# Kernel optimization log

Measured on AMD Instinct MI355X. Metric: run time of the kernel, lower is better.

Reference implementation:

```python
import jax, jax.numpy as jnp
import numpy as np

TOP_K = 2


def setup_inputs() -> dict:
    key = jax.random.key(0)
    ks = jax.random.split(key, 5)
    B, S, H, F, E = 1, 2048, 1024, 3584, 8
    scale_h = 1.0 / np.sqrt(H)
    scale_f = 1.0 / np.sqrt(F)
    return {
        "hidden_states": jax.random.normal(ks[0], (B, S, H), dtype=jnp.float32),
        "gate_w": jax.random.normal(ks[1], (E, H), dtype=jnp.float32) * scale_h,
        "w1": jax.random.normal(ks[2], (E, H, F), dtype=jnp.float32) * scale_h,
        "w3": jax.random.normal(ks[3], (E, H, F), dtype=jnp.float32) * scale_h,
        "w2": jax.random.normal(ks[4], (E, F, H), dtype=jnp.float32) * scale_f,
    }


def reference(hidden_states, gate_w, w1, w2, w3):
    B, S, H = hidden_states.shape
    E = gate_w.shape[0]
    x = hidden_states.reshape(-1, H)  # [T, H]
    # Router: logits -> fp32 softmax -> top-k -> renormalize
    router_logits = x @ gate_w.T  # [T, E]
    probs = jax.nn.softmax(router_logits.astype(jnp.float32), axis=-1)
    top_w, top_idx = jax.lax.top_k(probs, TOP_K)  # [T, K]
    top_w = top_w / jnp.sum(top_w, axis=-1, keepdims=True)
    top_w = top_w.astype(x.dtype)
    # Dense combine weights [T, E]: routing weight if expert selected else 0
    combine = jnp.sum(jax.nn.one_hot(top_idx, E, dtype=x.dtype) * top_w[..., None], axis=1)
    # Per-expert SwiGLU FFN, weighted-summed (loop over small fixed E)
    out = jnp.zeros_like(x)
    for e in range(E):
        h = jax.nn.silu(x @ w1[e]) * (x @ w3[e])  # [T, F]
        out = out + (h @ w2[e]) * combine[:, e:e + 1]
    return out.reshape(B, S, H), router_logits
```

## Files before the change

### kernel.cpp

```cpp
#include <hip/hip_runtime.h>
#include <cstdint>
#include <cstddef>

#define Tt 2048
#define Hh 1024
#define Ff 3584
#define Ee 8
#define ROWS_CAP 5120

#define OFF_CTRL   0u
#define OFF_TOKE   256u
#define OFF_TOKW   (256u + 16384u)
#define OFF_ROWMAP (256u + 32768u)
#define OFF_ROWW   (256u + 32768u + 20480u)
#define OFF_XG     (1ull << 20)
#define OFF_G      (12ull << 20)
#define OFF_W1T    (48ull << 20)
#define OFF_W3T    (104ull << 20)
#define OFF_W2T    (160ull << 20)

typedef __attribute__((ext_vector_type(8))) short bf16x8;
typedef __attribute__((ext_vector_type(4))) float f32x4;

__device__ __forceinline__ unsigned short f2bf(float f) {
  unsigned int u = __float_as_uint(f);
  u += 0x7fffu + ((u >> 16) & 1u);
  return (unsigned short)(u >> 16);
}

__device__ __forceinline__ void gload_lds16(const void* g, void* l) {
  auto gp = (const __attribute__((address_space(1))) char*)(uintptr_t)g;
  auto lp = (__attribute__((address_space(3))) char*)(uintptr_t)l;
  __builtin_amdgcn_global_load_lds(gp, lp, 16, 0, 0);
}

__device__ __forceinline__ bf16x8 frg(const char* lds, int row, int gc) {
  return *(const bf16x8*)(lds + row * 64 + ((gc ^ ((row >> 1) & 3)) * 16));
}

__global__ __launch_bounds__(256) void router_kernel(
    const float* __restrict__ x, const float* __restrict__ gw,
    float* __restrict__ logits_out, int* __restrict__ tok_e,
    float* __restrict__ tok_w, int* __restrict__ ctrl) {
  const int lane = threadIdx.x & 63;
  const int t = blockIdx.x * 4 + (threadIdx.x >> 6);
  const float4* xp = (const float4*)(x + (size_t)t * Hh + lane * 16);
  float4 x0 = xp[0], x1 = xp[1], x2 = xp[2], x3 = xp[3];
  float lg[Ee];
#pragma unroll
  for (int e = 0; e < Ee; ++e) {
    const float4* gp = (const float4*)(gw + e * Hh + lane * 16);
    float4 g0 = gp[0], g1 = gp[1], g2 = gp[2], g3 = gp[3];
    float s = x0.x*g0.x + x0.y*g0.y + x0.z*g0.z + x0.w*g0.w
            + x1.x*g1.x + x1.y*g1.y + x1.z*g1.z + x1.w*g1.w
            + x2.x*g2.x + x2.y*g2.y + x2.z*g2.z + x2.w*g2.w
            + x3.x*g3.x + x3.y*g3.y + x3.z*g3.z + x3.w*g3.w;
#pragma unroll
    for (int o = 32; o; o >>= 1) s += __shfl_xor(s, o);
    lg[e] = s;
  }
  if (lane == 0) {
    float m = lg[0];
#pragma unroll
    for (int e = 1; e < Ee; ++e) m = fmaxf(m, lg[e]);
    float p[Ee];
#pragma unroll
    for (int e = 0; e < Ee; ++e) p[e] = expf(lg[e] - m);
    int a0 = 0;
#pragma unroll
    for (int e = 1; e < Ee; ++e) if (p[e] > p[a0]) a0 = e;
    int a1 = (a0 == 0) ? 1 : 0;
#pragma unroll
    for (int e = 0; e < Ee; ++e) if (e != a0 && p[e] > p[a1]) a1 = e;
    float rs = p[a0] + p[a1];
    float w0 = p[a0] / rs, w1 = p[a1] / rs;
#pragma unroll
    for (int e = 0; e < Ee; ++e) logits_out[(size_t)t * Ee + e] = lg[e];
    tok_e[t * 2] = a0; tok_e[t * 2 + 1] = a1;
    tok_w[t * 2] = w0; tok_w[t * 2 + 1] = w1;
    atomicAdd(&ctrl[a0], 1); atomicAdd(&ctrl[a1], 1);
  }
}

__global__ void offsets_kernel(int* ctrl) {
  if (threadIdx.x == 0) {
    int acc = 0;
    for (int e = 0; e < Ee; ++e) {
      ctrl[16 + e] = acc;
      acc += ((ctrl[e] + 127) >> 7) << 7;
    }
    ctrl[16 + Ee] = acc;
  }
}

__global__ __launch_bounds__(512) void assign_kernel(
    int* ctrl, const int* __restrict__ tok_e, const float* __restrict__ tok_w,
    int* __restrict__ rowmap, float* __restrict__ roww) {
  int i = blockIdx.x * 512 + threadIdx.x;
  if (i < 2 * Tt) {
    int e = tok_e[i];
    int pos = atomicAdd(&ctrl[8 + e], 1);
    int r = ctrl[16 + e] + pos;
    rowmap[r] = i >> 1;
    roww[r] = tok_w[i];
  }
  if (i < Ee * 128) {
    int e = i >> 7, pd = i & 127;
    int o = ctrl[16 + e], o1 = ctrl[16 + e + 1], c = ctrl[e];
    int r = o + c + pd;
    if (r < o1) { rowmap[r] = -1; roww[r] = 0.f; }
  }
}

__global__ __launch_bounds__(128) void gather_kernel(
    const float* __restrict__ x, const int* __restrict__ ctrl,
    const int* __restrict__ rowmap, unsigned short* __restrict__ Xg) {
  int r = blockIdx.x;
  if (r >= ctrl[16 + Ee]) return;
  int t = rowmap[r];
  int j = threadIdx.x;
  uint4 v = make_uint4(0u, 0u, 0u, 0u);
  if (t >= 0) {
    const float4* xp = (const float4*)(x + (size_t)t * Hh + j * 8);
    float4 a = xp[0], b = xp[1];
    v.x = (unsigned)f2bf(a.x) | ((unsigned)f2bf(a.y) << 16);
    v.y = (unsigned)f2bf(a.z) | ((unsigned)f2bf(a.w) << 16);
    v.z = (unsigned)f2bf(b.x) | ((unsigned)f2bf(b.y) << 16);
    v.w = (unsigned)f2bf(b.z) | ((unsigned)f2bf(b.w) << 16);
  }
  *(uint4*)(Xg + (size_t)r * Hh + j * 8) = v;
}

__global__ __launch_bounds__(256) void tc_all(
    const float* __restrict__ w1, const float* __restrict__ w3,
    const float* __restrict__ w2, unsigned short* __restrict__ w1T,
    unsigned short* __restrict__ w3T, unsigned short* __restrict__ w2T) {
  __shared__ unsigned short sT[64 * 72];
  const int z = blockIdx.z;
  const float* in = (z == 0) ? w1 : (z == 1) ? w3 : w2;
  unsigned short* out = (z == 0) ? w1T : (z == 1) ? w3T : w2T;
  const int C = (z == 2) ? Hh : Ff;
  const int tiles_c = (z == 2) ? 16 : 56;
  const int R = (z == 2) ? Ff : Hh;
  const int e = blockIdx.y;
  const int tr = blockIdx.x / tiles_c, tc = blockIdx.x % tiles_c;
  const int r0 = tr * 64, c0 = tc * 64;
  const float* src = in + (size_t)e * R * C;
  unsigned short* dst = out + (size_t)e * R * C;
  const int t = threadIdx.x;
#pragma unroll
  for (int p = 0; p < 4; ++p) {
    int row = p * 16 + (t >> 4);
    float4 v = *(const float4*)(src + (size_t)(r0 + row) * C + c0 + (t & 15) * 4);
    int cl = (t & 15) * 4;
    sT[(cl + 0) * 72 + row] = f2bf(v.x);
    sT[(cl + 1) * 72 + row] = f2bf(v.y);
    sT[(cl + 2) * 72 + row] = f2bf(v.z);
    sT[(cl + 3) * 72 + row] = f2bf(v.w);
  }
  __syncthreads();
  const int oc = t >> 2, half = t & 3;
  uint4 u0 = *(const uint4*)&sT[oc * 72 + half * 16];
  uint4 u1 = *(const uint4*)&sT[oc * 72 + half * 16 + 8];
  unsigned short* op = dst + (size_t)(c0 + oc) * R + r0 + half * 16;
  *(uint4*)op = u0;
  *(uint4*)(op + 8) = u1;
}

__global__ __launch_bounds__(512, 4) void ffn13_bf16(
    const unsigned short* __restrict__ Xg, const unsigned short* __restrict__ w1T,
    const unsigned short* __restrict__ w3T, const int* __restrict__ ctrl,
    unsigned short* __restrict__ G) {
  __shared__ alignas(16) char sA[2][8192], sB1[2][8192], sB3[2][8192];
  int lin = blockIdx.y * 28 + blockIdx.x;
  int wg = (lin & 7) * 448 + (lin >> 3);
  int bx = wg % 28, by = wg / 28;
  const int e = by >> 4, mt = by & 15;
  const int off0 = ctrl[16 + e], off1 = ctrl[16 + e + 1];
  const int row0 = off0 + mt * 128;
  if (row0 >= off1) return;
  const int n0 = bx * 128;
  const int tid = threadIdx.x, lane = tid & 63, wv = tid >> 6;
  const int wr = wv >> 2, wc = wv & 3;
  const unsigned short* w1e = w1T + (size_t)e * Ff * Hh;
  const unsigned short* w3e = w3T + (size_t)e * Ff * Hh;
  f32x4 acc1[4][2] = {};
  f32x4 acc3[4][2] = {};
  const int srow = wv * 16 + (lane >> 2);
  const int sgc = (lane & 3) ^ ((lane >> 3) & 3);
  const int swb = wv * 16;

  {
    size_t so = (size_t)sgc * 8;
    gload_lds16(Xg + (size_t)(row0 + srow) * Hh + so, sA[0] + swb * 64);
    gload_lds16(w1e + (size_t)(n0 + srow) * Hh + so, sB1[0] + swb * 64);
    gload_lds16(w3e + (size_t)(n0 + srow) * Hh + so, sB3[0] + swb * 64);
  }
  __syncthreads();
  for (int it = 0; it < 32; ++it) {
    int cur = it & 1;
    if (it < 31) {
      size_t so = (size_t)(it + 1) * 32 + sgc * 8;
      gload_lds16(Xg + (size_t)(row0 + srow) * Hh + so, sA[cur ^ 1] + swb * 64);
      gload_lds16(w1e + (size_t)(n0 + srow) * Hh + so, sB1[cur ^ 1] + swb * 64);
      gload_lds16(w3e + (size_t)(n0 + srow) * Hh + so, sB3[cur ^ 1] + swb * 64);
    }
    const int gc = lane >> 4;
    bf16x8 af[4];
#pragma unroll
    for (int mi = 0; mi < 4; ++mi)
      af[mi] = frg(sA[cur], wr * 64 + mi * 16 + (lane & 15), gc);
    __builtin_amdgcn_s_setprio(1);
#pragma unroll
    for (int ni = 0; ni < 2; ++ni) {
      bf16x8 b1 = frg(sB1[cur], wc * 32 + ni * 16 + (lane & 15), gc);
      bf16x8 b3 = frg(sB3[cur], wc * 32 + ni * 16 + (lane & 15), gc);
#pragma unroll
      for (int mi = 0; mi < 4; ++mi) {
        acc1[mi][ni] = __builtin_amdgcn_mfma_f32_16x16x32_bf16(af[mi], b1, acc1[mi][ni], 0, 0, 0);
        acc3[mi][ni] = __builtin_amdgcn_mfma_f32_16x16x32_bf16(af[mi], b3, acc3[mi][ni], 0, 0, 0);
      }
    }
    __builtin_amdgcn_s_setprio(0);
    __syncthreads();
  }
  const int rb = wr * 64 + 4 * (lane >> 4), cb = wc * 32 + (lane & 15);
#pragma unroll
  for (int mi = 0; mi < 4; ++mi)
#pragma unroll
    for (int ni = 0; ni < 2; ++ni)
#pragma unroll
      for (int r = 0; r < 4; ++r) {
        float h1 = acc1[mi][ni][r], h3 = acc3[mi][ni][r];
        float gv = h1 / (1.f + __expf(-h1)) * h3;
        G[(size_t)(row0 + rb + mi * 16 + r) * Ff + n0 + cb + ni * 16] = f2bf(gv);
      }
}

__global__ __launch_bounds__(256, 4) void ffn2_bf16(
    const unsigned short* __restrict__ G, const unsigned short* __restrict__ w2T,
    const int* __restrict__ ctrl, const int* __restrict__ rowmap,
    const float* __restrict__ roww, float* __restrict__ out) {
  __shared__ alignas(16) char sA[2][8192], sB[2][8192];
  int lin = blockIdx.y * 8 + blockIdx.x;
  int wg = (lin & 7) * 128 + (lin >> 3);
  int bx = wg % 8, by = wg / 8;
  const int e = by >> 4, mt = by & 15;
  const int off0 = ctrl[16 + e], off1 = ctrl[16 + e + 1];
  const int row0 = off0 + mt * 128;
  if (row0 >= off1) return;
  const int n0 = bx * 128;
  const int kb = blockIdx.z * (Ff / 4);
  const int tid = threadIdx.x, lane = tid & 63, wv = tid >> 6;
  const int wr = wv >> 1, wc = wv & 1;
  const unsigned short* w2e = w2T + (size_t)e * Ff * Hh;
  f32x4 acc[4][4] = {};
  const int sl = lane >> 2;
  const int sgc = (lane & 3) ^ ((lane >> 3) & 3);

#pragma unroll
  for (int half = 0; half < 2; ++half) {
    int wb = wv * 16 + half * 64;
    size_t so = (size_t)kb + sgc * 8;
    gload_lds16(G + (size_t)(row0 + wb + sl) * Ff + so, sA[0] + wb * 64);
    gload_lds16(w2e + (size_t)(n0 + wb + sl) * Ff + so, sB[0] + wb * 64);
  }
  __syncthreads();
  for (int it = 0; it < 28; ++it) {
    int cur = it & 1;
    if (it < 27) {
#pragma unroll
      for (int half = 0; half < 2; ++half) {
        int wb = wv * 16 + half * 64;
        size_t so = (size_t)kb + (it + 1) * 32 + sgc * 8;
        gload_lds16(G + (size_t)(row0 + wb + sl) * Ff + so, sA[cur ^ 1] + wb * 64);
        gload_lds16(w2e + (size_t)(n0 + wb + sl) * Ff + so, sB[cur ^ 1] + wb * 64);
      }
    }
    const int gc = lane >> 4;
    bf16x8 af[4];
#pragma unroll
    for (int mi = 0; mi < 4; ++mi)
      af[mi] = frg(sA[cur], wr * 64 + mi * 16 + (lane & 15), gc);
    __builtin_amdgcn_s_setprio(1);
#pragma unroll
    for (int ni = 0; ni < 4; ++ni) {
      bf16x8 b = frg(sB[cur], wc * 64 + ni * 16 + (lane & 15), gc);
#pragma unroll
      for (int mi = 0; mi < 4; ++mi)
        acc[mi][ni] = __builtin_amdgcn_mfma_f32_16x16x32_bf16(af[mi], b, acc[mi][ni], 0, 0, 0);
    }
    __builtin_amdgcn_s_setprio(0);
    __syncthreads();
  }
  const int rb = wr * 64 + 4 * (lane >> 4), cb = wc * 64 + (lane & 15);
#pragma unroll
  for (int mi = 0; mi < 4; ++mi)
#pragma unroll
    for (int r = 0; r < 4; ++r) {
      int grow = row0 + rb + mi * 16 + r;
      int t = rowmap[grow];
      if (t < 0) continue;
      float wgt = roww[grow];
#pragma unroll
      for (int ni = 0; ni < 4; ++ni)
        atomicAdd(&out[(size_t)t * Hh + n0 + cb + ni * 16], wgt * acc[mi][ni][r]);
    }
}

extern "C" void kernel_launch(void* const* d_in, const int* in_sizes, int n_in,
                              void* d_out, int out_size, void* d_ws, size_t ws_size,
                              hipStream_t stream) {
  const float* x  = (const float*)d_in[0];
  const float* gw = (const float*)d_in[1];
  const float* w1 = (const float*)d_in[2];
  const float* w3 = (const float*)d_in[3];
  const float* w2 = (const float*)d_in[4];
  float* out = (float*)d_out;
  float* logits = out + (size_t)Tt * Hh;
  char* ws = (char*)d_ws;
  int* ctrl = (int*)(ws + OFF_CTRL);
  int* tok_e = (int*)(ws + OFF_TOKE);
  float* tok_w = (float*)(ws + OFF_TOKW);
  int* rowmap = (int*)(ws + OFF_ROWMAP);
  float* roww = (float*)(ws + OFF_ROWW);
  unsigned short* Xg = (unsigned short*)(ws + OFF_XG);
  unsigned short* G  = (unsigned short*)(ws + OFF_G);
  unsigned short* w1T = (unsigned short*)(ws + OFF_W1T);
  unsigned short* w3T = (unsigned short*)(ws + OFF_W3T);
  unsigned short* w2T = (unsigned short*)(ws + OFF_W2T);

  hipMemsetAsync(ctrl, 0, 256, stream);
  hipMemsetAsync(out, 0, (size_t)Tt * Hh * sizeof(float), stream);
  router_kernel<<<Tt / 4, 256, 0, stream>>>(x, gw, logits, tok_e, tok_w, ctrl);
  offsets_kernel<<<1, 64, 0, stream>>>(ctrl);
  assign_kernel<<<8, 512, 0, stream>>>(ctrl, tok_e, tok_w, rowmap, roww);
  gather_kernel<<<ROWS_CAP, 128, 0, stream>>>(x, ctrl, rowmap, Xg);
  tc_all<<<dim3(896, Ee, 3), 256, 0, stream>>>(w1, w3, w2, w1T, w3T, w2T);
  ffn13_bf16<<<dim3(28, Ee * 16), 512, 0, stream>>>(Xg, w1T, w3T, ctrl, G);
  ffn2_bf16<<<dim3(8, Ee * 16, 4), 256, 0, stream>>>(G, w2T, ctrl, rowmap, roww, out);
}
```

Before: 372.8 us.

## Use partial vmcnt waits in GEMM loops and swizzle transpose LDS tile

The GEMM main loops of both FFN kernels now issue next-tile async global-to-LDS loads before waiting. They wait only with a partial s_waitcnt vmcnt so the current tile's loads complete while the prefetch stays in flight. Full __syncthreads are replaced by raw s_barrier plus sched_barrier, and the last iteration issues a dummy wraparound prefetch to keep the loop branch-free. Separately, the weight transpose kernel packs four rows per thread into 8-byte LDS stores with an XOR swizzle, cutting scalar 2-byte shared stores and bank conflicts. The risk is subtle ordering bugs and extra wasted loads at loop end.

```diff
diff --git a/kernel.cpp b/kernel.cpp
--- a/kernel.cpp
+++ b/kernel.cpp
@@ -135,7 +135,7 @@
     const float* __restrict__ w1, const float* __restrict__ w3,
     const float* __restrict__ w2, unsigned short* __restrict__ w1T,
     unsigned short* __restrict__ w3T, unsigned short* __restrict__ w2T) {
-  __shared__ unsigned short sT[64 * 72];
+  __shared__ alignas(16) char sT[64 * 128];
   const int z = blockIdx.z;
   const float* in = (z == 0) ? w1 : (z == 1) ? w3 : w2;
   unsigned short* out = (z == 0) ? w1T : (z == 1) ? w3T : w2T;
@@ -148,23 +148,35 @@
   const float* src = in + (size_t)e * R * C;
   unsigned short* dst = out + (size_t)e * R * C;
   const int t = threadIdx.x;
-#pragma unroll
-  for (int p = 0; p < 4; ++p) {
-    int row = p * 16 + (t >> 4);
-    float4 v = *(const float4*)(src + (size_t)(r0 + row) * C + c0 + (t & 15) * 4);
-    int cl = (t & 15) * 4;
-    sT[(cl + 0) * 72 + row] = f2bf(v.x);
-    sT[(cl + 1) * 72 + row] = f2bf(v.y);
-    sT[(cl + 2) * 72 + row] = f2bf(v.z);
-    sT[(cl + 3) * 72 + row] = f2bf(v.w);
+
+  const int col4 = (t & 15) * 4, rb = (t >> 4) * 4;
+  float4 v0 = *(const float4*)(src + (size_t)(r0 + rb + 0) * C + c0 + col4);
+  float4 v1 = *(const float4*)(src + (size_t)(r0 + rb + 1) * C + c0 + col4);
+  float4 v2 = *(const float4*)(src + (size_t)(r0 + rb + 2) * C + c0 + col4);
+  float4 v3 = *(const float4*)(src + (size_t)(r0 + rb + 3) * C + c0 + col4);
+  const float* a0 = (const float*)&v0;
+  const float* a1 = (const float*)&v1;
+  const float* a2 = (const float*)&v2;
+  const float* a3 = (const float*)&v3;
+#pragma unroll
+  for (int j = 0; j < 4; ++j) {
+    int c = col4 + j;
+    int M = (((c & 7) ^ ((c >> 3) & 7)) << 4);
+    uint2 val;
+    val.x = (unsigned)f2bf(a0[j]) | ((unsigned)f2bf(a1[j]) << 16);
+    val.y = (unsigned)f2bf(a2[j]) | ((unsigned)f2bf(a3[j]) << 16);
+    *(uint2*)(sT + c * 128 + ((rb * 2) ^ M)) = val;
   }
   __syncthreads();
-  const int oc = t >> 2, half = t & 3;
-  uint4 u0 = *(const uint4*)&sT[oc * 72 + half * 16];
-  uint4 u1 = *(const uint4*)&sT[oc * 72 + half * 16 + 8];
-  unsigned short* op = dst + (size_t)(c0 + oc) * R + r0 + half * 16;
-  *(uint4*)op = u0;
-  *(uint4*)(op + 8) = u1;
+  const int lane = t & 63, wv = t >> 6;
+  const int h8 = lane >> 3;
+#pragma unroll
+  for (int p = 0; p < 2; ++p) {
+    int c = p * 32 + wv * 8 + (lane & 7);
+    int M = (((c & 7) ^ ((c >> 3) & 7)) << 4);
+    uint4 q = *(const uint4*)(sT + c * 128 + ((h8 * 16) ^ M));
+    *(uint4*)(dst + (size_t)(c0 + c) * R + r0 + h8 * 8) = q;
+  }
 }
 
 __global__ __launch_bounds__(512, 4) void ffn13_bf16(
@@ -190,21 +202,24 @@
   const int sgc = (lane & 3) ^ ((lane >> 3) & 3);
   const int swb = wv * 16;
 
-  {
-    size_t so = (size_t)sgc * 8;
-    gload_lds16(Xg + (size_t)(row0 + srow) * Hh + so, sA[0] + swb * 64);
-    gload_lds16(w1e + (size_t)(n0 + srow) * Hh + so, sB1[0] + swb * 64);
-    gload_lds16(w3e + (size_t)(n0 + srow) * Hh + so, sB3[0] + swb * 64);
-  }
-  __syncthreads();
+  const unsigned short* gA = Xg + (size_t)(row0 + srow) * Hh + sgc * 8;
+  const unsigned short* gB1 = w1e + (size_t)(n0 + srow) * Hh + sgc * 8;
+  const unsigned short* gB3 = w3e + (size_t)(n0 + srow) * Hh + sgc * 8;
+
+  gload_lds16(gA, sA[0] + swb * 64);
+  gload_lds16(gB1, sB1[0] + swb * 64);
+  gload_lds16(gB3, sB3[0] + swb * 64);
+
   for (int it = 0; it < 32; ++it) {
     int cur = it & 1;
-    if (it < 31) {
-      size_t so = (size_t)(it + 1) * 32 + sgc * 8;
-      gload_lds16(Xg + (size_t)(row0 + srow) * Hh + so, sA[cur ^ 1] + swb * 64);
-      gload_lds16(w1e + (size_t)(n0 + srow) * Hh + so, sB1[cur ^ 1] + swb * 64);
-      gload_lds16(w3e + (size_t)(n0 + srow) * Hh + so, sB3[cur ^ 1] + swb * 64);
-    }
+    int nx = it + 1; if (nx == 32) nx = 0;
+    size_t so = (size_t)nx * 32;
+    gload_lds16(gA + so, sA[cur ^ 1] + swb * 64);
+    gload_lds16(gB1 + so, sB1[cur ^ 1] + swb * 64);
+    gload_lds16(gB3 + so, sB3[cur ^ 1] + swb * 64);
+    asm volatile("s_waitcnt vmcnt(3)" ::: "memory");
+    __builtin_amdgcn_s_barrier();
+    __builtin_amdgcn_sched_barrier(0);
     const int gc = lane >> 4;
     bf16x8 af[4];
 #pragma unroll
@@ -222,8 +237,10 @@
       }
     }
     __builtin_amdgcn_s_setprio(0);
-    __syncthreads();
-  }
+    __builtin_amdgcn_sched_barrier(0);
+    __builtin_amdgcn_s_barrier();
+  }
+  asm volatile("s_waitcnt vmcnt(0)" ::: "memory");
   const int rb = wr * 64 + 4 * (lane >> 4), cb = wc * 32 + (lane & 15);
 #pragma unroll
   for (int mi = 0; mi < 4; ++mi)
@@ -258,25 +275,27 @@
   const int sl = lane >> 2;
   const int sgc = (lane & 3) ^ ((lane >> 3) & 3);
 
-#pragma unroll
-  for (int half = 0; half < 2; ++half) {
-    int wb = wv * 16 + half * 64;
-    size_t so = (size_t)kb + sgc * 8;
-    gload_lds16(G + (size_t)(row0 + wb + sl) * Ff + so, sA[0] + wb * 64);
-    gload_lds16(w2e + (size_t)(n0 + wb + sl) * Ff + so, sB[0] + wb * 64);
-  }
-  __syncthreads();
+  const unsigned short* gA0 = G + (size_t)(row0 + wv * 16 + sl) * Ff + kb + sgc * 8;
+  const unsigned short* gA1 = G + (size_t)(row0 + 64 + wv * 16 + sl) * Ff + kb + sgc * 8;
+  const unsigned short* gB0 = w2e + (size_t)(n0 + wv * 16 + sl) * Ff + kb + sgc * 8;
+  const unsigned short* gB1 = w2e + (size_t)(n0 + 64 + wv * 16 + sl) * Ff + kb + sgc * 8;
+
+  gload_lds16(gA0, sA[0] + (wv * 16) * 64);
+  gload_lds16(gA1, sA[0] + (wv * 16 + 64) * 64);
+  gload_lds16(gB0, sB[0] + (wv * 16) * 64);
+  gload_lds16(gB1, sB[0] + (wv * 16 + 64) * 64);
+
   for (int it = 0; it < 28; ++it) {
     int cur = it & 1;
-    if (it < 27) {
-#pragma unroll
-      for (int half = 0; half < 2; ++half) {
-        int wb = wv * 16 + half * 64;
-        size_t so = (size_t)kb + (it + 1) * 32 + sgc * 8;
-        gload_lds16(G + (size_t)(row0 + wb + sl) * Ff + so, sA[cur ^ 1] + wb * 64);
-        gload_lds16(w2e + (size_t)(n0 + wb + sl) * Ff + so, sB[cur ^ 1] + wb * 64);
-      }
-    }
+    int nx = it + 1; if (nx == 28) nx = 0;
+    size_t so = (size_t)nx * 32;
+    gload_lds16(gA0 + so, sA[cur ^ 1] + (wv * 16) * 64);
+    gload_lds16(gA1 + so, sA[cur ^ 1] + (wv * 16 + 64) * 64);
+    gload_lds16(gB0 + so, sB[cur ^ 1] + (wv * 16) * 64);
+    gload_lds16(gB1 + so, sB[cur ^ 1] + (wv * 16 + 64) * 64);
+    asm volatile("s_waitcnt vmcnt(4)" ::: "memory");
+    __builtin_amdgcn_s_barrier();
+    __builtin_amdgcn_sched_barrier(0);
     const int gc = lane >> 4;
     bf16x8 af[4];
 #pragma unroll
@@ -291,8 +310,10 @@
         acc[mi][ni] = __builtin_amdgcn_mfma_f32_16x16x32_bf16(af[mi], b, acc[mi][ni], 0, 0, 0);
     }
     __builtin_amdgcn_s_setprio(0);
-    __syncthreads();
-  }
+    __builtin_amdgcn_sched_barrier(0);
+    __builtin_amdgcn_s_barrier();
+  }
+  asm volatile("s_waitcnt vmcnt(0)" ::: "memory");
   const int rb = wr * 64 + 4 * (lane >> 4), cb = wc * 64 + (lane & 15);
 #pragma unroll
   for (int mi = 0; mi < 4; ++mi)
```

Measured after the change: 367.1 us. No clear change (-1.5%).

## Fuse fp32 weight conversion into expert GEMMs and drop transpose pass

Applied to the files above, without the earlier changes.

Removes the separate kernel that converted and transposed all expert weights to bf16 each call. Both FFN GEMMs now read fp32 weights straight from the original layout, pack them to bf16 in registers with v_cvt_pk_bf16_f32, and store them into swizzled LDS while the current tile's MFMAs run. The down-projection also drops its 4-way K split: it runs 512 threads with 112 K iterations and half as many output columns per wave. This saves a full read-and-write pass over the weights, at the cost of strided fp32 global loads and more weight traffic from reloads across M tiles and less parallelism in the second GEMM.

```diff
diff --git a/kernel.cpp b/kernel.cpp
--- a/kernel.cpp
+++ b/kernel.cpp
@@ -15,9 +15,6 @@
 #define OFF_ROWW   (256u + 32768u + 20480u)
 #define OFF_XG     (1ull << 20)
 #define OFF_G      (12ull << 20)
-#define OFF_W1T    (48ull << 20)
-#define OFF_W3T    (104ull << 20)
-#define OFF_W2T    (160ull << 20)
 
 typedef __attribute__((ext_vector_type(8))) short bf16x8;
 typedef __attribute__((ext_vector_type(4))) float f32x4;
@@ -26,6 +23,12 @@
   unsigned int u = __float_as_uint(f);
   u += 0x7fffu + ((u >> 16) & 1u);
   return (unsigned short)(u >> 16);
+}
+
+__device__ __forceinline__ unsigned pkbf(float a, float b) {
+  unsigned r;
+  asm("v_cvt_pk_bf16_f32 %0, %1, %2" : "=v"(r) : "v"(a), "v"(b));
+  return r;
 }
 
 __device__ __forceinline__ void gload_lds16(const void* g, void* l) {
@@ -131,45 +134,9 @@
   *(uint4*)(Xg + (size_t)r * Hh + j * 8) = v;
 }
 
-__global__ __launch_bounds__(256) void tc_all(
-    const float* __restrict__ w1, const float* __restrict__ w3,
-    const float* __restrict__ w2, unsigned short* __restrict__ w1T,
-    unsigned short* __restrict__ w3T, unsigned short* __restrict__ w2T) {
-  __shared__ unsigned short sT[64 * 72];
-  const int z = blockIdx.z;
-  const float* in = (z == 0) ? w1 : (z == 1) ? w3 : w2;
-  unsigned short* out = (z == 0) ? w1T : (z == 1) ? w3T : w2T;
-  const int C = (z == 2) ? Hh : Ff;
-  const int tiles_c = (z == 2) ? 16 : 56;
-  const int R = (z == 2) ? Ff : Hh;
-  const int e = blockIdx.y;
-  const int tr = blockIdx.x / tiles_c, tc = blockIdx.x % tiles_c;
-  const int r0 = tr * 64, c0 = tc * 64;
-  const float* src = in + (size_t)e * R * C;
-  unsigned short* dst = out + (size_t)e * R * C;
-  const int t = threadIdx.x;
-#pragma unroll
-  for (int p = 0; p < 4; ++p) {
-    int row = p * 16 + (t >> 4);
-    float4 v = *(const float4*)(src + (size_t)(r0 + row) * C + c0 + (t & 15) * 4);
-    int cl = (t & 15) * 4;
-    sT[(cl + 0) * 72 + row] = f2bf(v.x);
-    sT[(cl + 1) * 72 + row] = f2bf(v.y);
-    sT[(cl + 2) * 72 + row] = f2bf(v.z);
-    sT[(cl + 3) * 72 + row] = f2bf(v.w);
-  }
-  __syncthreads();
-  const int oc = t >> 2, half = t & 3;
-  uint4 u0 = *(const uint4*)&sT[oc * 72 + half * 16];
-  uint4 u1 = *(const uint4*)&sT[oc * 72 + half * 16 + 8];
-  unsigned short* op = dst + (size_t)(c0 + oc) * R + r0 + half * 16;
-  *(uint4*)op = u0;
-  *(uint4*)(op + 8) = u1;
-}
-
-__global__ __launch_bounds__(512, 4) void ffn13_bf16(
-    const unsigned short* __restrict__ Xg, const unsigned short* __restrict__ w1T,
-    const unsigned short* __restrict__ w3T, const int* __restrict__ ctrl,
+__global__ __launch_bounds__(512, 4) void ffn13_fused(
+    const unsigned short* __restrict__ Xg, const float* __restrict__ w1,
+    const float* __restrict__ w3, const int* __restrict__ ctrl,
     unsigned short* __restrict__ G) {
   __shared__ alignas(16) char sA[2][8192], sB1[2][8192], sB3[2][8192];
   int lin = blockIdx.y * 28 + blockIdx.x;
@@ -182,28 +149,47 @@
   const int n0 = bx * 128;
   const int tid = threadIdx.x, lane = tid & 63, wv = tid >> 6;
   const int wr = wv >> 2, wc = wv & 3;
-  const unsigned short* w1e = w1T + (size_t)e * Ff * Hh;
-  const unsigned short* w3e = w3T + (size_t)e * Ff * Hh;
+  const float* w1e = w1 + (size_t)e * Hh * Ff;
+  const float* w3e = w3 + (size_t)e * Hh * Ff;
   f32x4 acc1[4][2] = {};
   f32x4 acc3[4][2] = {};
   const int srow = wv * 16 + (lane >> 2);
   const int sgc = (lane & 3) ^ ((lane >> 3) & 3);
-  const int swb = wv * 16;
-
+  const unsigned short* gA = Xg + (size_t)(row0 + srow) * Hh + sgc * 8;
+  const int bn = tid & 127, bkq = tid >> 7;
+  const int posB = bkq ^ ((bn >> 1) & 3);
+  const int wofB = bn * 64 + posB * 16;
+  const float* pB1 = w1e + (size_t)(bkq * 8) * Ff + n0 + bn;
+  const float* pB3 = w3e + (size_t)(bkq * 8) * Ff + n0 + bn;
+  float r1[8], r3[8];
+
+#pragma unroll
+  for (int i = 0; i < 8; ++i) r1[i] = pB1[(size_t)i * Ff];
+#pragma unroll
+  for (int i = 0; i < 8; ++i) r3[i] = pB3[(size_t)i * Ff];
+  gload_lds16(gA, sA[0] + wv * 1024);
   {
-    size_t so = (size_t)sgc * 8;
-    gload_lds16(Xg + (size_t)(row0 + srow) * Hh + so, sA[0] + swb * 64);
-    gload_lds16(w1e + (size_t)(n0 + srow) * Hh + so, sB1[0] + swb * 64);
-    gload_lds16(w3e + (size_t)(n0 + srow) * Hh + so, sB3[0] + swb * 64);
+    uint4 q;
+    q.x = pkbf(r1[0], r1[1]); q.y = pkbf(r1[2], r1[3]);
+    q.z = pkbf(r1[4], r1[5]); q.w = pkbf(r1[6], r1[7]);
+    *(uint4*)(sB1[0] + wofB) = q;
+    q.x = pkbf(r3[0], r3[1]); q.y = pkbf(r3[2], r3[3]);
+    q.z = pkbf(r3[4], r3[5]); q.w = pkbf(r3[6], r3[7]);
+    *(uint4*)(sB3[0] + wofB) = q;
   }
   __syncthreads();
+
   for (int it = 0; it < 32; ++it) {
-    int cur = it & 1;
+    const int cur = it & 1;
     if (it < 31) {
-      size_t so = (size_t)(it + 1) * 32 + sgc * 8;
-      gload_lds16(Xg + (size_t)(row0 + srow) * Hh + so, sA[cur ^ 1] + swb * 64);
-      gload_lds16(w1e + (size_t)(n0 + srow) * Hh + so, sB1[cur ^ 1] + swb * 64);
-      gload_lds16(w3e + (size_t)(n0 + srow) * Hh + so, sB3[cur ^ 1] + swb * 64);
+      const size_t ko = (size_t)(it + 1) * 32;
+      gload_lds16(gA + ko, sA[cur ^ 1] + wv * 1024);
+      const float* p1 = pB1 + ko * Ff;
+      const float* p3 = pB3 + ko * Ff;
+#pragma unroll
+      for (int i = 0; i < 8; ++i) r1[i] = p1[(size_t)i * Ff];
+#pragma unroll
+      for (int i = 0; i < 8; ++i) r3[i] = p3[(size_t)i * Ff];
     }
     const int gc = lane >> 4;
     bf16x8 af[4];
@@ -222,6 +208,15 @@
       }
     }
     __builtin_amdgcn_s_setprio(0);
+    if (it < 31) {
+      uint4 q;
+      q.x = pkbf(r1[0], r1[1]); q.y = pkbf(r1[2], r1[3]);
+      q.z = pkbf(r1[4], r1[5]); q.w = pkbf(r1[6], r1[7]);
+      *(uint4*)(sB1[cur ^ 1] + wofB) = q;
+      q.x = pkbf(r3[0], r3[1]); q.y = pkbf(r3[2], r3[3]);
+      q.z = pkbf(r3[4], r3[5]); q.w = pkbf(r3[6], r3[7]);
+      *(uint4*)(sB3[cur ^ 1] + wofB) = q;
+    }
     __syncthreads();
   }
   const int rb = wr * 64 + 4 * (lane >> 4), cb = wc * 32 + (lane & 15);
@@ -237,8 +232,8 @@
       }
 }
 
-__global__ __launch_bounds__(256, 4) void ffn2_bf16(
-    const unsigned short* __restrict__ G, const unsigned short* __restrict__ w2T,
+__global__ __launch_bounds__(512, 4) void ffn2_fused(
+    const unsigned short* __restrict__ G, const float* __restrict__ w2,
     const int* __restrict__ ctrl, const int* __restrict__ rowmap,
     const float* __restrict__ roww, float* __restrict__ out) {
   __shared__ alignas(16) char sA[2][8192], sB[2][8192];
@@ -250,32 +245,38 @@
   const int row0 = off0 + mt * 128;
   if (row0 >= off1) return;
   const int n0 = bx * 128;
-  const int kb = blockIdx.z * (Ff / 4);
   const int tid = threadIdx.x, lane = tid & 63, wv = tid >> 6;
-  const int wr = wv >> 1, wc = wv & 1;
-  const unsigned short* w2e = w2T + (size_t)e * Ff * Hh;
-  f32x4 acc[4][4] = {};
-  const int sl = lane >> 2;
+  const int wr = wv >> 2, wc = wv & 3;
+  const float* w2e = w2 + (size_t)e * Ff * Hh;
+  f32x4 acc[4][2] = {};
+  const int srow = wv * 16 + (lane >> 2);
   const int sgc = (lane & 3) ^ ((lane >> 3) & 3);
-
-#pragma unroll
-  for (int half = 0; half < 2; ++half) {
-    int wb = wv * 16 + half * 64;
-    size_t so = (size_t)kb + sgc * 8;
-    gload_lds16(G + (size_t)(row0 + wb + sl) * Ff + so, sA[0] + wb * 64);
-    gload_lds16(w2e + (size_t)(n0 + wb + sl) * Ff + so, sB[0] + wb * 64);
+  const unsigned short* gA = G + (size_t)(row0 + srow) * Ff + sgc * 8;
+  const int bn = tid & 127, bkq = tid >> 7;
+  const int posB = bkq ^ ((bn >> 1) & 3);
+  const int wofB = bn * 64 + posB * 16;
+  const float* pB = w2e + (size_t)(bkq * 8) * Hh + n0 + bn;
+  float r2[8];
+
+#pragma unroll
+  for (int i = 0; i < 8; ++i) r2[i] = pB[(size_t)i * Hh];
+  gload_lds16(gA, sA[0] + wv * 1024);
+  {
+    uint4 q;
+    q.x = pkbf(r2[0], r2[1]); q.y = pkbf(r2[2], r2[3]);
+    q.z = pkbf(r2[4], r2[5]); q.w = pkbf(r2[6], r2[7]);
+    *(uint4*)(sB[0] + wofB) = q;
   }
   __syncthreads();
-  for (int it = 0; it < 28; ++it) {
-    int cur = it & 1;
-    if (it < 27) {
-#pragma unroll
-      for (int half = 0; half < 2; ++half) {
-        int wb = wv * 16 + half * 64;
-        size_t so = (size_t)kb + (it + 1) * 32 + sgc * 8;
-        gload_lds16(G + (size_t)(row0 + wb + sl) * Ff + so, sA[cur ^ 1] + wb * 64);
-        gload_lds16(w2e + (size_t)(n0 + wb + sl) * Ff + so, sB[cur ^ 1] + wb * 64);
-      }
+
+  for (int it = 0; it < 112; ++it) {
+    const int cur = it & 1;
+    if (it < 111) {
+      const size_t ko = (size_t)(it + 1) * 32;
+      gload_lds16(gA + ko, sA[cur ^ 1] + wv * 1024);
+      const float* p2 = pB + ko * Hh;
+#pragma unroll
+      for (int i = 0; i < 8; ++i) r2[i] = p2[(size_t)i * Hh];
     }
     const int gc = lane >> 4;
     bf16x8 af[4];
@@ -284,16 +285,22 @@
       af[mi] = frg(sA[cur], wr * 64 + mi * 16 + (lane & 15), gc);
     __builtin_amdgcn_s_setprio(1);
 #pragma unroll
-    for (int ni = 0; ni < 4; ++ni) {
-      bf16x8 b = frg(sB[cur], wc * 64 + ni * 16 + (lane & 15), gc);
+    for (int ni = 0; ni < 2; ++ni) {
+      bf16x8 b = frg(sB[cur], wc * 32 + ni * 16 + (lane & 15), gc);
 #pragma unroll
       for (int mi = 0; mi < 4; ++mi)
         acc[mi][ni] = __builtin_amdgcn_mfma_f32_16x16x32_bf16(af[mi], b, acc[mi][ni], 0, 0, 0);
     }
     __builtin_amdgcn_s_setprio(0);
+    if (it < 111) {
+      uint4 q;
+      q.x = pkbf(r2[0], r2[1]); q.y = pkbf(r2[2], r2[3]);
+      q.z = pkbf(r2[4], r2[5]); q.w = pkbf(r2[6], r2[7]);
+      *(uint4*)(sB[cur ^ 1] + wofB) = q;
+    }
     __syncthreads();
   }
-  const int rb = wr * 64 + 4 * (lane >> 4), cb = wc * 64 + (lane & 15);
+  const int rb = wr * 64 + 4 * (lane >> 4), cb = wc * 32 + (lane & 15);
 #pragma unroll
   for (int mi = 0; mi < 4; ++mi)
 #pragma unroll
@@ -303,7 +310,7 @@
       if (t < 0) continue;
       float wgt = roww[grow];
 #pragma unroll
-      for (int ni = 0; ni < 4; ++ni)
+      for (int ni = 0; ni < 2; ++ni)
         atomicAdd(&out[(size_t)t * Hh + n0 + cb + ni * 16], wgt * acc[mi][ni][r]);
     }
 }
@@ -326,9 +333,6 @@
   float* roww = (float*)(ws + OFF_ROWW);
   unsigned short* Xg = (unsigned short*)(ws + OFF_XG);
   unsigned short* G  = (unsigned short*)(ws + OFF_G);
-  unsigned short* w1T = (unsigned short*)(ws + OFF_W1T);
-  unsigned short* w3T = (unsigned short*)(ws + OFF_W3T);
-  unsigned short* w2T = (unsigned short*)(ws + OFF_W2T);
 
   hipMemsetAsync(ctrl, 0, 256, stream);
   hipMemsetAsync(out, 0, (size_t)Tt * Hh * sizeof(float), stream);
@@ -336,7 +340,6 @@
   offsets_kernel<<<1, 64, 0, stream>>>(ctrl);
   assign_kernel<<<8, 512, 0, stream>>>(ctrl, tok_e, tok_w, rowmap, roww);
   gather_kernel<<<ROWS_CAP, 128, 0, stream>>>(x, ctrl, rowmap, Xg);
-  tc_all<<<dim3(896, Ee, 3), 256, 0, stream>>>(w1, w3, w2, w1T, w3T, w2T);
-  ffn13_bf16<<<dim3(28, Ee * 16), 512, 0, stream>>>(Xg, w1T, w3T, ctrl, G);
-  ffn2_bf16<<<dim3(8, Ee * 16, 4), 256, 0, stream>>>(G, w2T, ctrl, rowmap, roww, out);
-}
+  ffn13_fused<<<dim3(28, Ee * 16), 512, 0, stream>>>(Xg, w1, w3, ctrl, G);
+  ffn2_fused<<<dim3(8, Ee * 16), 512, 0, stream>>>(G, w2, ctrl, rowmap, roww, out);
+}
```

Result: faster. 344.8 us (-7.5%).

## Compact expert tile schedule, widen weight transpose tiles, retile ffn2 to 512 threads

Applied to the files above, without the earlier changes.

The offsets kernel now builds a compact list of up to 40 (expert, row-tile) pairs, so both GEMMs launch only about 40 row tiles instead of 128 mostly-empty slots with early exits. The weight transpose/convert kernel now handles 128x64 tiles per block, uses packed bf16 conversion and an XOR-swizzled LDS layout, and halves its block count. ffn2 moves to 512 threads with a 32-column warp tile. This removes wasted block launches and scheduling gaps, at the cost of a fixed MAXT cap on row tiles.

```diff
diff --git a/kernel.cpp b/kernel.cpp
--- a/kernel.cpp
+++ b/kernel.cpp
@@ -7,17 +7,18 @@
 #define Ff 3584
 #define Ee 8
 #define ROWS_CAP 5120
+#define MAXT 40
 
 #define OFF_CTRL   0u
-#define OFF_TOKE   256u
-#define OFF_TOKW   (256u + 16384u)
-#define OFF_ROWMAP (256u + 32768u)
-#define OFF_ROWW   (256u + 32768u + 20480u)
-#define OFF_XG     (1ull << 20)
-#define OFF_G      (12ull << 20)
-#define OFF_W1T    (48ull << 20)
-#define OFF_W3T    (104ull << 20)
-#define OFF_W2T    (160ull << 20)
+#define OFF_TOKE   4096u
+#define OFF_TOKW   (4096u + 16384u)
+#define OFF_ROWMAP 65536u
+#define OFF_ROWW   98304u
+#define OFF_XG     262144ull
+#define OFF_G      10747904ull
+#define OFF_W1T    47448064ull
+#define OFF_W3T    106168320ull
+#define OFF_W2T    164888576ull
 
 typedef __attribute__((ext_vector_type(8))) short bf16x8;
 typedef __attribute__((ext_vector_type(4))) float f32x4;
@@ -26,6 +27,12 @@
   unsigned int u = __float_as_uint(f);
   u += 0x7fffu + ((u >> 16) & 1u);
   return (unsigned short)(u >> 16);
+}
+
+__device__ __forceinline__ unsigned pkbf(float a, float b) {
+  unsigned r;
+  asm("v_cvt_pk_bf16_f32 %0, %1, %2" : "=v"(r) : "v"(a), "v"(b));
+  return r;
 }
 
 __device__ __forceinline__ void gload_lds16(const void* g, void* l) {
@@ -90,6 +97,16 @@
       acc += ((ctrl[e] + 127) >> 7) << 7;
     }
     ctrl[16 + Ee] = acc;
+    int idx = 0;
+    for (int e = 0; e < Ee; ++e) {
+      int nt = (ctrl[e] + 127) >> 7;
+      for (int m = 0; m < nt && idx < MAXT; ++m) {
+        ctrl[32 + 2 * idx] = e;
+        ctrl[33 + 2 * idx] = ctrl[16 + e] + m * 128;
+        ++idx;
+      }
+    }
+    for (; idx < MAXT; ++idx) { ctrl[32 + 2 * idx] = 0; ctrl[33 + 2 * idx] = -1; }
   }
 }
 
@@ -135,50 +152,59 @@
     const float* __restrict__ w1, const float* __restrict__ w3,
     const float* __restrict__ w2, unsigned short* __restrict__ w1T,
     unsigned short* __restrict__ w3T, unsigned short* __restrict__ w2T) {
-  __shared__ unsigned short sT[64 * 72];
+  __shared__ alignas(16) char sT[64 * 256];
   const int z = blockIdx.z;
   const float* in = (z == 0) ? w1 : (z == 1) ? w3 : w2;
   unsigned short* out = (z == 0) ? w1T : (z == 1) ? w3T : w2T;
+  const int R = (z == 2) ? Ff : Hh;
   const int C = (z == 2) ? Hh : Ff;
   const int tiles_c = (z == 2) ? 16 : 56;
-  const int R = (z == 2) ? Ff : Hh;
   const int e = blockIdx.y;
-  const int tr = blockIdx.x / tiles_c, tc = blockIdx.x % tiles_c;
-  const int r0 = tr * 64, c0 = tc * 64;
+  const int tr = blockIdx.x / tiles_c, tcc = blockIdx.x % tiles_c;
+  const int r0g = tr * 128, c0 = tcc * 64;
   const float* src = in + (size_t)e * R * C;
   unsigned short* dst = out + (size_t)e * R * C;
   const int t = threadIdx.x;
-#pragma unroll
-  for (int p = 0; p < 4; ++p) {
-    int row = p * 16 + (t >> 4);
-    float4 v = *(const float4*)(src + (size_t)(r0 + row) * C + c0 + (t & 15) * 4);
-    int cl = (t & 15) * 4;
-    sT[(cl + 0) * 72 + row] = f2bf(v.x);
-    sT[(cl + 1) * 72 + row] = f2bf(v.y);
-    sT[(cl + 2) * 72 + row] = f2bf(v.z);
-    sT[(cl + 3) * 72 + row] = f2bf(v.w);
+
+  const int col4 = (t & 15) * 4, rb = (t >> 4) * 8;
+  float4 v[8];
+#pragma unroll
+  for (int i = 0; i < 8; ++i)
+    v[i] = *(const float4*)(src + (size_t)(r0g + rb + i) * C + c0 + col4);
+#pragma unroll
+  for (int j = 0; j < 4; ++j) {
+    const float* a = (const float*)&v[0];
+    int c = col4 + j;
+    int M = (((c & 7) ^ ((c >> 3) & 7)) << 4);
+    uint4 q;
+    q.x = pkbf(((const float*)&v[0])[j], ((const float*)&v[1])[j]);
+    q.y = pkbf(((const float*)&v[2])[j], ((const float*)&v[3])[j]);
+    q.z = pkbf(((const float*)&v[4])[j], ((const float*)&v[5])[j]);
+    q.w = pkbf(((const float*)&v[6])[j], ((const float*)&v[7])[j]);
+    (void)a;
+    *(uint4*)(sT + c * 256 + ((rb * 2) ^ M)) = q;
   }
   __syncthreads();
-  const int oc = t >> 2, half = t & 3;
-  uint4 u0 = *(const uint4*)&sT[oc * 72 + half * 16];
-  uint4 u1 = *(const uint4*)&sT[oc * 72 + half * 16 + 8];
-  unsigned short* op = dst + (size_t)(c0 + oc) * R + r0 + half * 16;
-  *(uint4*)op = u0;
-  *(uint4*)(op + 8) = u1;
-}
-
-__global__ __launch_bounds__(512, 4) void ffn13_bf16(
+  const int oc = t >> 2, part = t & 3;
+  const int M = (((oc & 7) ^ ((oc >> 3) & 7)) << 4);
+#pragma unroll
+  for (int i = 0; i < 4; ++i) {
+    uint4 q = *(const uint4*)(sT + oc * 256 + ((i * 64 + part * 16) ^ M));
+    *(uint4*)(dst + (size_t)(c0 + oc) * R + r0g + i * 32 + part * 8) = q;
+  }
+}
+
+__global__ __launch_bounds__(512, 4) void h13_gemm(
     const unsigned short* __restrict__ Xg, const unsigned short* __restrict__ w1T,
     const unsigned short* __restrict__ w3T, const int* __restrict__ ctrl,
     unsigned short* __restrict__ G) {
   __shared__ alignas(16) char sA[2][8192], sB1[2][8192], sB3[2][8192];
   int lin = blockIdx.y * 28 + blockIdx.x;
-  int wg = (lin & 7) * 448 + (lin >> 3);
-  int bx = wg % 28, by = wg / 28;
-  const int e = by >> 4, mt = by & 15;
-  const int off0 = ctrl[16 + e], off1 = ctrl[16 + e + 1];
-  const int row0 = off0 + mt * 128;
-  if (row0 >= off1) return;
+  int wg = (lin & 7) * 140 + (lin >> 3);
+  int ft = wg % 40, bx = wg / 40;
+  const int e = ctrl[32 + 2 * ft];
+  const int row0 = ctrl[33 + 2 * ft];
+  if (row0 < 0) return;
   const int n0 = bx * 128;
   const int tid = threadIdx.x, lane = tid & 63, wv = tid >> 6;
   const int wr = wv >> 2, wc = wv & 3;
@@ -188,22 +214,22 @@
   f32x4 acc3[4][2] = {};
   const int srow = wv * 16 + (lane >> 2);
   const int sgc = (lane & 3) ^ ((lane >> 3) & 3);
-  const int swb = wv * 16;
-
-  {
-    size_t so = (size_t)sgc * 8;
-    gload_lds16(Xg + (size_t)(row0 + srow) * Hh + so, sA[0] + swb * 64);
-    gload_lds16(w1e + (size_t)(n0 + srow) * Hh + so, sB1[0] + swb * 64);
-    gload_lds16(w3e + (size_t)(n0 + srow) * Hh + so, sB3[0] + swb * 64);
-  }
+  const unsigned short* gA  = Xg  + (size_t)(row0 + srow) * Hh + sgc * 8;
+  const unsigned short* gB1 = w1e + (size_t)(n0 + srow) * Hh + sgc * 8;
+  const unsigned short* gB3 = w3e + (size_t)(n0 + srow) * Hh + sgc * 8;
+
+  gload_lds16(gA,  sA[0]  + wv * 1024);
+  gload_lds16(gB1, sB1[0] + wv * 1024);
+  gload_lds16(gB3, sB3[0] + wv * 1024);
   __syncthreads();
+
   for (int it = 0; it < 32; ++it) {
-    int cur = it & 1;
+    const int cur = it & 1;
     if (it < 31) {
-      size_t so = (size_t)(it + 1) * 32 + sgc * 8;
-      gload_lds16(Xg + (size_t)(row0 + srow) * Hh + so, sA[cur ^ 1] + swb * 64);
-      gload_lds16(w1e + (size_t)(n0 + srow) * Hh + so, sB1[cur ^ 1] + swb * 64);
-      gload_lds16(w3e + (size_t)(n0 + srow) * Hh + so, sB3[cur ^ 1] + swb * 64);
+      const size_t ko = (size_t)(it + 1) * 32;
+      gload_lds16(gA + ko,  sA[cur ^ 1]  + wv * 1024);
+      gload_lds16(gB1 + ko, sB1[cur ^ 1] + wv * 1024);
+      gload_lds16(gB3 + ko, sB3[cur ^ 1] + wv * 1024);
     }
     const int gc = lane >> 4;
     bf16x8 af[4];
@@ -237,45 +263,40 @@
       }
 }
 
-__global__ __launch_bounds__(256, 4) void ffn2_bf16(
+__global__ __launch_bounds__(512, 4) void ffn2_gemm(
     const unsigned short* __restrict__ G, const unsigned short* __restrict__ w2T,
     const int* __restrict__ ctrl, const int* __restrict__ rowmap,
     const float* __restrict__ roww, float* __restrict__ out) {
   __shared__ alignas(16) char sA[2][8192], sB[2][8192];
-  int lin = blockIdx.y * 8 + blockIdx.x;
-  int wg = (lin & 7) * 128 + (lin >> 3);
-  int bx = wg % 8, by = wg / 8;
-  const int e = by >> 4, mt = by & 15;
-  const int off0 = ctrl[16 + e], off1 = ctrl[16 + e + 1];
-  const int row0 = off0 + mt * 128;
-  if (row0 >= off1) return;
+  int lin = (blockIdx.z * MAXT + blockIdx.y) * 8 + blockIdx.x;
+  int wg = (lin & 7) * 160 + (lin >> 3);
+  int ft = wg % 40, q = wg / 40;
+  int bx = q & 7, ks = q >> 3;
+  const int e = ctrl[32 + 2 * ft];
+  const int row0 = ctrl[33 + 2 * ft];
+  if (row0 < 0) return;
   const int n0 = bx * 128;
-  const int kb = blockIdx.z * (Ff / 4);
+  const int kb = ks * (Ff / 4);
   const int tid = threadIdx.x, lane = tid & 63, wv = tid >> 6;
-  const int wr = wv >> 1, wc = wv & 1;
+  const int wr = wv >> 2, wc = wv & 3;
   const unsigned short* w2e = w2T + (size_t)e * Ff * Hh;
-  f32x4 acc[4][4] = {};
-  const int sl = lane >> 2;
+  f32x4 acc[4][2] = {};
+  const int srow = wv * 16 + (lane >> 2);
   const int sgc = (lane & 3) ^ ((lane >> 3) & 3);
-
-#pragma unroll
-  for (int half = 0; half < 2; ++half) {
-    int wb = wv * 16 + half * 64;
-    size_t so = (size_t)kb + sgc * 8;
-    gload_lds16(G + (size_t)(row0 + wb + sl) * Ff + so, sA[0] + wb * 64);
-    gload_lds16(w2e + (size_t)(n0 + wb + sl) * Ff + so, sB[0] + wb * 64);
-  }
+  const unsigned short* gA = G   + (size_t)(row0 + srow) * Ff + kb + sgc * 8;
+  const unsigned short* gB = w2e + (size_t)(n0 + srow) * Ff + kb + sgc * 8;
+
+  gload_lds16(gA, sA[0] + wv * 1024);
+  gload_lds16(gB, sB[0] + wv * 1024);
   __syncthreads();
-  for (int it = 0; it < 28; ++it) {
-    int cur = it & 1;
-    if (it < 27) {
-#pragma unroll
-      for (int half = 0; half < 2; ++half) {
-        int wb = wv * 16 + half * 64;
-        size_t so = (size_t)kb + (it + 1) * 32 + sgc * 8;
-        gload_lds16(G + (size_t)(row0 + wb + sl) * Ff + so, sA[cur ^ 1] + wb * 64);
-        gload_lds16(w2e + (size_t)(n0 + wb + sl) * Ff + so, sB[cur ^ 1] + wb * 64);
-      }
+
+  const int NT = 28;
+  for (int it = 0; it < NT; ++it) {
+    const int cur = it & 1;
+    if (it < NT - 1) {
+      const size_t ko = (size_t)(it + 1) * 32;
+      gload_lds16(gA + ko, sA[cur ^ 1] + wv * 1024);
+      gload_lds16(gB + ko, sB[cur ^ 1] + wv * 1024);
     }
     const int gc = lane >> 4;
     bf16x8 af[4];
@@ -284,8 +305,8 @@
       af[mi] = frg(sA[cur], wr * 64 + mi * 16 + (lane & 15), gc);
     __builtin_amdgcn_s_setprio(1);
 #pragma unroll
-    for (int ni = 0; ni < 4; ++ni) {
-      bf16x8 b = frg(sB[cur], wc * 64 + ni * 16 + (lane & 15), gc);
+    for (int ni = 0; ni < 2; ++ni) {
+      bf16x8 b = frg(sB[cur], wc * 32 + ni * 16 + (lane & 15), gc);
 #pragma unroll
       for (int mi = 0; mi < 4; ++mi)
         acc[mi][ni] = __builtin_amdgcn_mfma_f32_16x16x32_bf16(af[mi], b, acc[mi][ni], 0, 0, 0);
@@ -293,7 +314,7 @@
     __builtin_amdgcn_s_setprio(0);
     __syncthreads();
   }
-  const int rb = wr * 64 + 4 * (lane >> 4), cb = wc * 64 + (lane & 15);
+  const int rb = wr * 64 + 4 * (lane >> 4), cb = wc * 32 + (lane & 15);
 #pragma unroll
   for (int mi = 0; mi < 4; ++mi)
 #pragma unroll
@@ -303,7 +324,7 @@
       if (t < 0) continue;
       float wgt = roww[grow];
 #pragma unroll
-      for (int ni = 0; ni < 4; ++ni)
+      for (int ni = 0; ni < 2; ++ni)
         atomicAdd(&out[(size_t)t * Hh + n0 + cb + ni * 16], wgt * acc[mi][ni][r]);
     }
 }
@@ -324,19 +345,19 @@
   float* tok_w = (float*)(ws + OFF_TOKW);
   int* rowmap = (int*)(ws + OFF_ROWMAP);
   float* roww = (float*)(ws + OFF_ROWW);
-  unsigned short* Xg = (unsigned short*)(ws + OFF_XG);
-  unsigned short* G  = (unsigned short*)(ws + OFF_G);
+  unsigned short* Xg  = (unsigned short*)(ws + OFF_XG);
+  unsigned short* G   = (unsigned short*)(ws + OFF_G);
   unsigned short* w1T = (unsigned short*)(ws + OFF_W1T);
   unsigned short* w3T = (unsigned short*)(ws + OFF_W3T);
   unsigned short* w2T = (unsigned short*)(ws + OFF_W2T);
 
-  hipMemsetAsync(ctrl, 0, 256, stream);
+  hipMemsetAsync(ctrl, 0, 512, stream);
   hipMemsetAsync(out, 0, (size_t)Tt * Hh * sizeof(float), stream);
   router_kernel<<<Tt / 4, 256, 0, stream>>>(x, gw, logits, tok_e, tok_w, ctrl);
   offsets_kernel<<<1, 64, 0, stream>>>(ctrl);
   assign_kernel<<<8, 512, 0, stream>>>(ctrl, tok_e, tok_w, rowmap, roww);
   gather_kernel<<<ROWS_CAP, 128, 0, stream>>>(x, ctrl, rowmap, Xg);
-  tc_all<<<dim3(896, Ee, 3), 256, 0, stream>>>(w1, w3, w2, w1T, w3T, w2T);
-  ffn13_bf16<<<dim3(28, Ee * 16), 512, 0, stream>>>(Xg, w1T, w3T, ctrl, G);
-  ffn2_bf16<<<dim3(8, Ee * 16, 4), 256, 0, stream>>>(G, w2T, ctrl, rowmap, roww, out);
-}
+  tc_all<<<dim3(448, Ee, 3), 256, 0, stream>>>(w1, w3, w2, w1T, w3T, w2T);
+  h13_gemm<<<dim3(28, MAXT), 512, 0, stream>>>(Xg, w1T, w3T, ctrl, G);
+  ffn2_gemm<<<dim3(8, MAXT, 4), 512, 0, stream>>>(G, w2T, ctrl, rowmap, roww, out);
+}
```

New measurement: 366.5 us. No clear change (-1.7%).
